# Performance work log

Measured on AMD Instinct MI355X. Metric: run time of the kernel, lower is better.

The kernel has to match this reference:

```python
import jax, jax.numpy as jnp
import numpy as np

DIM = 1024
N_HEADS = 16
HEAD_DIM = DIM // N_HEADS
SPARSITY = 0.8
SCALE = HEAD_DIM ** -0.5


def setup_inputs() -> dict:
    key = jax.random.key(0)
    ks = jax.random.split(key, 9)
    B, S = 2, 2048
    std = DIM ** -0.5
    return {
        "x": jax.random.normal(ks[0], (B, S, DIM), dtype=jnp.float32),
        "wq": jax.random.normal(ks[1], (DIM, DIM), dtype=jnp.float32) * std,
        "bq": jnp.zeros((DIM,), dtype=jnp.float32),
        "wk": jax.random.normal(ks[2], (DIM, DIM), dtype=jnp.float32) * std,
        "bk": jnp.zeros((DIM,), dtype=jnp.float32),
        "wv": jax.random.normal(ks[3], (DIM, DIM), dtype=jnp.float32) * std,
        "bv": jnp.zeros((DIM,), dtype=jnp.float32),
        "wo": jax.random.normal(ks[4], (DIM, DIM), dtype=jnp.float32) * std,
        "bo": jnp.zeros((DIM,), dtype=jnp.float32),
    }


def _attn(x, wq, bq, wk, bk, wv, bv, wo, bo):
    B, S, _ = x.shape
    # torch Linear: y = x @ W.T + b
    def proj(w, b):
        y = jnp.einsum('bsd,ed->bse', x, w) + b
        return y.reshape(B, S, N_HEADS, HEAD_DIM).transpose(0, 2, 1, 3)  # [B,H,S,hd]
    q, k, v = proj(wq, bq), proj(wk, bk), proj(wv, bv)
    scores = jnp.einsum('bhqd,bhkd->bhqk', q, k) * SCALE  # [B,H,S,S]
    # top-k sparsity: keep k = max(1, int(S*(1-sparsity))) largest per row
    kk = max(1, int(S * (1.0 - SPARSITY)))
    topk_vals, topk_idx = jax.lax.top_k(scores, kk)
    sparse = jnp.full_like(scores, -jnp.inf)
    sparse = jnp.put_along_axis(sparse, topk_idx, topk_vals, axis=-1, inplace=False)
    attn = jax.nn.softmax(sparse, axis=-1)  # dropout disabled (eval)
    out = jnp.einsum('bhqk,bhkd->bhqd', attn, v)
    out = out.transpose(0, 2, 1, 3).reshape(B, S, DIM)
    out = jnp.einsum('bsd,ed->bse', out, wo) + bo
    return out, attn


def reference(x, wq, bq, wk, bk, wv, bv, wo, bo):
    return _attn(x, wq, bq, wk, bk, wv, bv, wo, bo)
```

## Files before the change

kernel.cpp:

```cpp
#include <hip/hip_runtime.h>
#include <hip/hip_bf16.h>

#define DIMN 1024
#define NH 16
#define HD 64
#define SEQ 2048
#define BATCH 2
#define BHN (BATCH*NH)
#define MROWS (BATCH*SEQ)
#define KKEEP 409
#define SCALEF 0.125f
#define QROWS 16

typedef __attribute__((ext_vector_type(8))) short short8;
typedef __attribute__((ext_vector_type(4))) short short4v;
typedef __attribute__((ext_vector_type(4))) float f32x4;

#define MFMA(a,b,c) __builtin_amdgcn_mfma_f32_16x16x32_bf16(a,b,c,0,0,0)


static __device__ __forceinline__ short f2bf(float f) {
    __hip_bfloat16 h = __float2bfloat16(f);
    return *reinterpret_cast<short*>(&h);
}
static __device__ __forceinline__ float bf2f(short s) {
    __hip_bfloat16 h = *reinterpret_cast<__hip_bfloat16*>(&s);
    return __bfloat162float(h);
}
static __device__ __forceinline__ short8 ld8(const short* p) {
    return *reinterpret_cast<const short8*>(p);
}
static __device__ __forceinline__ float keyf(unsigned u) {
    unsigned fu = (u & 0x80000000u) ? (u ^ 0x80000000u) : ~u;
    return __uint_as_float(fu);
}
static __device__ __forceinline__ size_t tidx(int row, int k) {
    return (size_t)(row >> 4) * 16384 + (size_t)(k >> 5) * 512
         + ((((k >> 3) & 3) * 16 + (row & 15)) * 8) + (k & 7);
}

static __device__ __forceinline__ void conv_hilo_body(
    const float* in, short* hi, short* lo, int rows) {
    const int total = rows * 256;
    for (int idx = blockIdx.x * blockDim.x + threadIdx.x; idx < total;
         idx += gridDim.x * blockDim.x) {
        const int row = idx >> 8;
        const int k = (idx & 255) * 4;
        float4 v = *reinterpret_cast<const float4*>(in + (size_t)row * DIMN + k);
        short4v h, l;
        #pragma unroll
        for (int j = 0; j < 4; ++j) {
            float f = (&v.x)[j];
            short hb = f2bf(f);
            h[j] = hb;
            l[j] = f2bf(f - bf2f(hb));
        }
        const size_t o = tidx(row, k);
        *reinterpret_cast<short4v*>(hi + o) = h;
        *reinterpret_cast<short4v*>(lo + o) = l;
    }
}
static __device__ __forceinline__ void conv_bf16_body(
    const float* in, short* out, int rows) {
    const int total = rows * 256;
    for (int idx = blockIdx.x * blockDim.x + threadIdx.x; idx < total;
         idx += gridDim.x * blockDim.x) {
        const int row = idx >> 8;
        const int k = (idx & 255) * 4;
        float4 v = *reinterpret_cast<const float4*>(in + (size_t)row * DIMN + k);
        short4v o;
        o[0] = f2bf(v.x); o[1] = f2bf(v.y); o[2] = f2bf(v.z); o[3] = f2bf(v.w);
        *reinterpret_cast<short4v*>(out + tidx(row, k)) = o;
    }
}
__global__ void conv_all(
    const float* __restrict__ x, const float* __restrict__ wq,
    const float* __restrict__ wk, const float* __restrict__ wv,
    const float* __restrict__ wo,
    short* __restrict__ xhi, short* __restrict__ xlo,
    short* __restrict__ wqh, short* __restrict__ wql,
    short* __restrict__ wkh, short* __restrict__ wkl,
    short* __restrict__ wvb, short* __restrict__ wob)
{
    switch (blockIdx.y) {
        case 0: conv_hilo_body(x,  xhi, xlo, MROWS); break;
        case 1: conv_hilo_body(wq, wqh, wql, DIMN);  break;
        case 2: conv_hilo_body(wk, wkh, wkl, DIMN);  break;
        case 3: conv_bf16_body(wv, wvb, DIMN);       break;
        default: conv_bf16_body(wo, wob, DIMN);      break;
    }
}

__global__ __launch_bounds__(256) void qkv_mfma(
    const short* __restrict__ xh, const short* __restrict__ xl,
    const short* __restrict__ wqh, const short* __restrict__ wql, const float* __restrict__ bq,
    const short* __restrict__ wkh, const short* __restrict__ wkl, const float* __restrict__ bk,
    const short* __restrict__ wvb, const float* __restrict__ bv,
    short* __restrict__ qhi, short* __restrict__ qlo,
    short* __restrict__ khi, short* __restrict__ klo,
    short* __restrict__ vt)
{
    const int z = blockIdx.z;
    const int tid  = threadIdx.x;
    const int wv_  = tid >> 6, lane = tid & 63;
    const int r    = lane & 15, kg = lane >> 4;
    const int m_base = blockIdx.x * 128 + wv_ * 32;
    const int n_base = blockIdx.y * 64;
    const int mtile0 = blockIdx.x * 8 + wv_ * 2;
    const int ntile0 = blockIdx.y * 4;
    const int h = blockIdx.y;

    f32x4 acc[2][4] = {};

    if (z < 2) {
        const short* wh = z ? wkh : wqh;
        const short* wl = z ? wkl : wql;
        const float* bias = z ? bk : bq;
        short* dhi = z ? khi : qhi;
        short* dlo = z ? klo : qlo;

        for (int ks = 0; ks < 32; ++ks) {
            short8 ah0 = ld8(xh + (size_t)mtile0 * 16384 + ks * 512 + lane * 8);
            short8 al0 = ld8(xl + (size_t)mtile0 * 16384 + ks * 512 + lane * 8);
            short8 ah1 = ld8(xh + (size_t)(mtile0 + 1) * 16384 + ks * 512 + lane * 8);
            short8 al1 = ld8(xl + (size_t)(mtile0 + 1) * 16384 + ks * 512 + lane * 8);
            #pragma unroll
            for (int nf = 0; nf < 4; ++nf) {
                short8 bh = ld8(wh + (size_t)(ntile0 + nf) * 16384 + ks * 512 + lane * 8);
                short8 bl = ld8(wl + (size_t)(ntile0 + nf) * 16384 + ks * 512 + lane * 8);
                acc[0][nf] = MFMA(ah0, bh, acc[0][nf]);
                acc[0][nf] = MFMA(ah0, bl, acc[0][nf]);
                acc[0][nf] = MFMA(al0, bh, acc[0][nf]);
                acc[1][nf] = MFMA(ah1, bh, acc[1][nf]);
                acc[1][nf] = MFMA(ah1, bl, acc[1][nf]);
                acc[1][nf] = MFMA(al1, bh, acc[1][nf]);
            }
        }

        #pragma unroll
        for (int mf = 0; mf < 2; ++mf)
            #pragma unroll
            for (int nf = 0; nf < 4; ++nf)
                #pragma unroll
                for (int i = 0; i < 4; ++i) {
                    const int m  = m_base + mf * 16 + kg * 4 + i;
                    const int nn = n_base + nf * 16 + r;
                    const float val = acc[mf][nf][i] + bias[nn];
                    const int b_ = m >> 11, s = m & 2047;
                    const int hd = nf * 16 + r;
                    const size_t idx = (size_t)(b_ * NH + h) * 131072
                        + (size_t)(s >> 4) * 1024 + (hd >> 5) * 512
                        + ((((hd >> 3) & 3) * 16 + (s & 15)) * 8) + (hd & 7);
                    const short hb = f2bf(val);
                    dhi[idx] = hb;
                    dlo[idx] = f2bf(val - bf2f(hb));
                }
    } else {
        for (int ks = 0; ks < 32; ++ks) {
            short8 ah0 = ld8(xh + (size_t)mtile0 * 16384 + ks * 512 + lane * 8);
            short8 al0 = ld8(xl + (size_t)mtile0 * 16384 + ks * 512 + lane * 8);
            short8 ah1 = ld8(xh + (size_t)(mtile0 + 1) * 16384 + ks * 512 + lane * 8);
            short8 al1 = ld8(xl + (size_t)(mtile0 + 1) * 16384 + ks * 512 + lane * 8);
            #pragma unroll
            for (int nf = 0; nf < 4; ++nf) {
                short8 b = ld8(wvb + (size_t)(ntile0 + nf) * 16384 + ks * 512 + lane * 8);
                acc[0][nf] = MFMA(ah0, b, acc[0][nf]);
                acc[0][nf] = MFMA(al0, b, acc[0][nf]);
                acc[1][nf] = MFMA(ah1, b, acc[1][nf]);
                acc[1][nf] = MFMA(al1, b, acc[1][nf]);
            }
        }

        #pragma unroll
        for (int mf = 0; mf < 2; ++mf)
            #pragma unroll
            for (int nf = 0; nf < 4; ++nf)
                #pragma unroll
                for (int i = 0; i < 4; ++i) {
                    const int m  = m_base + mf * 16 + kg * 4 + i;
                    const int nn = n_base + nf * 16 + r;
                    const float val = acc[mf][nf][i] + bv[nn];
                    const int b_ = m >> 11, s = m & 2047;
                    const int hd = nf * 16 + r;
                    const size_t idx = (size_t)(b_ * NH + h) * 131072
                        + (size_t)(hd >> 4) * 32768 + (size_t)(s >> 5) * 512
                        + ((((s >> 3) & 3) * 16 + (hd & 15)) * 8) + (s & 7);
                    vt[idx] = f2bf(val);
                }
    }
}

__global__ __launch_bounds__(512, 4) void fused_attn(
    const short* __restrict__ qh, const short* __restrict__ ql,
    const short* __restrict__ kh, const short* __restrict__ kl,
    const short* __restrict__ vtb, float* __restrict__ attn,
    short* __restrict__ ctxt)
{
    __shared__ __align__(16) char smem[65536];
    float* CT = (float*)(smem + 32768);

    const int tid = threadIdx.x;
    const int w   = tid >> 6, lane = tid & 63;
    const int r   = lane & 15, kg = lane >> 4;

    const int bid  = blockIdx.x;
    const int xcd  = bid & 7;
    const int slot = bid >> 3;
    const int bh   = xcd + 8 * (slot >> 7);
    const int qt   = slot & 127;
    const int q0   = qt * QROWS;

    const size_t qtbase = (size_t)bh * 131072 + (size_t)qt * 1024 + lane * 8;
    short8 a0h = ld8(qh + qtbase),       a0l = ld8(ql + qtbase);
    short8 a1h = ld8(qh + qtbase + 512), a1l = ld8(ql + qtbase + 512);

    unsigned u[2][32];

    auto STAGE = [&](int c, float* buf) {
        #pragma unroll
        for (int tt = 0; tt < 4; ++tt) {
            const int stile = c * 32 + w + 8 * tt;
            const size_t tb = (size_t)bh * 131072 + (size_t)stile * 1024 + lane * 8;
            short8 b0h = ld8(kh + tb);
            short8 b0l = ld8(kl + tb);
            short8 b1h = ld8(kh + tb + 512);
            short8 b1l = ld8(kl + tb + 512);
            f32x4 accA = {0.f, 0.f, 0.f, 0.f};
            f32x4 accB = {0.f, 0.f, 0.f, 0.f};
            accA = MFMA(a0h, b0h, accA);
            accB = MFMA(a1h, b1h, accB);
            accA = MFMA(a0h, b0l, accA);
            accB = MFMA(a1h, b1l, accB);
            accA = MFMA(a0l, b0h, accA);
            accB = MFMA(a1l, b1h, accB);
            const int j0c = (w + 8 * tt) * 16;
            #pragma unroll
            for (int i = 0; i < 4; ++i)
                buf[(kg * 4 + i) * 512 + j0c + r] = (accA[i] + accB[i]) * SCALEF;
        }
    };

    STAGE(0, (float*)smem);
    __syncthreads();
    #pragma unroll
    for (int c = 0; c < 4; ++c) {
        float* cur = (float*)(smem + ((c & 1) ? 32768 : 0));
        float* nxt = (float*)(smem + ((c & 1) ? 0 : 32768));
        if (c + 1 < 4) STAGE(c + 1, nxt);
        #pragma unroll
        for (int rr = 0; rr < 2; ++rr) {
            const float* src = cur + (w + 8 * rr) * 512;
            #pragma unroll
            for (int g = 0; g < 2; ++g) {
                f32x4 v4 = *reinterpret_cast<const f32x4*>(src + g * 256 + lane * 4);
                #pragma unroll
                for (int q_ = 0; q_ < 4; ++q_) {
                    unsigned fu = __float_as_uint(v4[q_]);
                    u[rr][c * 8 + g * 4 + q_] =
                        (fu & 0x80000000u) ? ~fu : (fu | 0x80000000u);
                }
            }
        }
        __syncthreads();
    }

    float inv[2];
    #pragma unroll
    for (int rr = 0; rr < 2; ++rr) {
        unsigned cur = 0;
        for (int bit = 31; bit >= 0; --bit) {
            const unsigned cand = cur | (1u << bit);
            int cnt = 0;
            #pragma unroll
            for (int jj = 0; jj < 32; ++jj)
                cnt += __popcll(__ballot(u[rr][jj] >= cand));
            if (cnt >= KKEEP) {
                cur = cand;
                if (cnt == KKEEP) break;
            }
        }
        unsigned mu = 0;
        #pragma unroll
        for (int jj = 0; jj < 32; ++jj) mu = (u[rr][jj] > mu) ? u[rr][jj] : mu;
        #pragma unroll
        for (int off = 32; off; off >>= 1) {
            unsigned o = (unsigned)__shfl_xor((int)mu, off);
            mu = (o > mu) ? o : mu;
        }
        const float m = keyf(mu);
        float denom = 0.f;
        #pragma unroll
        for (int jj = 0; jj < 32; ++jj) {
            const unsigned ue = u[rr][jj];
            const float e = (ue >= cur) ? __expf(keyf(ue) - m) : 0.f;
            u[rr][jj] = __float_as_uint(e);
            denom += e;
        }
        #pragma unroll
        for (int off = 32; off; off >>= 1) denom += __shfl_xor(denom, off);
        inv[rr] = 1.0f / denom;
    }

    const int khf = w >> 2;
    const int swzw = (w & 7) << 4;
    const int swzr = (r & 7) << 4;
    f32x4 acc = {0.f, 0.f, 0.f, 0.f};

    auto EWRITE = [&](int c, char* Ebase) {
        #pragma unroll
        for (int rr = 0; rr < 2; ++rr) {
            const int row = w + 8 * rr;
            const float iv = inv[rr];
            #pragma unroll
            for (int g = 0; g < 2; ++g) {
                short4v pb;
                pb[0] = f2bf(__uint_as_float(u[rr][c * 8 + g * 4 + 0]) * iv);
                pb[1] = f2bf(__uint_as_float(u[rr][c * 8 + g * 4 + 1]) * iv);
                pb[2] = f2bf(__uint_as_float(u[rr][c * 8 + g * 4 + 2]) * iv);
                pb[3] = f2bf(__uint_as_float(u[rr][c * 8 + g * 4 + 3]) * iv);
                *reinterpret_cast<short4v*>(
                    Ebase + row * 1024 + ((g * 512 + lane * 8) ^ swzw)) = pb;
            }
        }
    };
    auto PVSTEP = [&](int c, const char* Ebase) {
        const size_t vbase = (size_t)bh * 131072 + (size_t)(w & 3) * 32768
                           + (size_t)(c * 16 + khf * 8) * 512 + lane * 8;
        const char* Eb2 = Ebase + r * 1024;
        #pragma unroll
        for (int ks = 0; ks < 8; ++ks) {
            const int kk = khf * 8 + ks;
            short8 pa = *reinterpret_cast<const short8*>(
                Eb2 + ((kk * 64 + kg * 16) ^ swzr));
            short8 vb = ld8(vtb + vbase + ks * 512);
            acc = MFMA(pa, vb, acc);
        }
    };

    EWRITE(0, smem);
    __syncthreads();
    #pragma unroll
    for (int c = 0; c < 4; ++c) {
        char* curE = smem + ((c & 1) ? 16384 : 0);
        char* nxtE = smem + ((c & 1) ? 0 : 16384);
        if (c + 1 < 4) EWRITE(c + 1, nxtE);
        PVSTEP(c, curE);
        __syncthreads();
    }

    const int dt = w & 3;
    if (khf == 1) {
        #pragma unroll
        for (int i = 0; i < 4; ++i) CT[(kg * 4 + i) * 64 + dt * 16 + r] = acc[i];
    }
    __syncthreads();
    if (khf == 0) {
        const int b_ = bh >> 4, h = bh & 15;
        const size_t base = (size_t)(b_ * 128 + qt) * 16384
                          + (size_t)(h * 2 + (dt >> 1)) * 512;
        #pragma unroll
        for (int i = 0; i < 4; ++i) {
            const int lrow = kg * 4 + i;
            const float val = acc[i] + CT[lrow * 64 + dt * 16 + r];
            ctxt[base + ((((dt * 2 + (r >> 3)) & 3) * 16 + lrow) * 8) + (r & 7)]
                = f2bf(val);
        }
    }

    #pragma unroll
    for (int rr = 0; rr < 2; ++rr) {
        const int row = w + 8 * rr;
        const float iv = inv[rr];
        float* arow = attn + ((size_t)bh * SEQ + q0 + row) * SEQ + lane * 4;
        #pragma unroll
        for (int c = 0; c < 4; ++c)
            #pragma unroll
            for (int g = 0; g < 2; ++g) {
                f32x4 pv;
                pv[0] = __uint_as_float(u[rr][c * 8 + g * 4 + 0]) * iv;
                pv[1] = __uint_as_float(u[rr][c * 8 + g * 4 + 1]) * iv;
                pv[2] = __uint_as_float(u[rr][c * 8 + g * 4 + 2]) * iv;
                pv[3] = __uint_as_float(u[rr][c * 8 + g * 4 + 3]) * iv;
                __builtin_nontemporal_store(
                    pv, reinterpret_cast<f32x4*>(arow + c * 512 + g * 256));
            }
    }
}

__global__ __launch_bounds__(256) void out_mfma(
    const short* __restrict__ ctxt, const short* __restrict__ wob,
    const float* __restrict__ bo, float* __restrict__ out)
{
    const int tid = threadIdx.x;
    const int w_  = tid >> 6, lane = tid & 63;
    const int r   = lane & 15, kg = lane >> 4;
    const int m_base = blockIdx.x * 128 + w_ * 32;
    const int n_base = blockIdx.y * 64;
    const int mtile0 = blockIdx.x * 8 + w_ * 2;
    const int ntile0 = blockIdx.y * 4;

    f32x4 acc[2][4] = {};

    for (int ks = 0; ks < 32; ++ks) {
        short8 a0 = ld8(ctxt + (size_t)mtile0 * 16384 + ks * 512 + lane * 8);
        short8 a1 = ld8(ctxt + (size_t)(mtile0 + 1) * 16384 + ks * 512 + lane * 8);
        #pragma unroll
        for (int nf = 0; nf < 4; ++nf) {
            short8 b = ld8(wob + (size_t)(ntile0 + nf) * 16384 + ks * 512 + lane * 8);
            acc[0][nf] = MFMA(a0, b, acc[0][nf]);
            acc[1][nf] = MFMA(a1, b, acc[1][nf]);
        }
    }

    #pragma unroll
    for (int mf = 0; mf < 2; ++mf)
        #pragma unroll
        for (int nf = 0; nf < 4; ++nf)
            #pragma unroll
            for (int i = 0; i < 4; ++i) {
                const int m  = m_base + mf * 16 + kg * 4 + i;
                const int nn = n_base + nf * 16 + r;
                out[(size_t)m * DIMN + nn] = acc[mf][nf][i] + bo[nn];
            }
}

extern "C" void kernel_launch(void* const* d_in, const int* in_sizes, int n_in,
                              void* d_out, int out_size, void* d_ws, size_t ws_size,
                              hipStream_t stream) {
    const float* x  = (const float*)d_in[0];
    const float* wq = (const float*)d_in[1];
    const float* bq = (const float*)d_in[2];
    const float* wk = (const float*)d_in[3];
    const float* bk = (const float*)d_in[4];
    const float* wv = (const float*)d_in[5];
    const float* bv = (const float*)d_in[6];
    const float* wo = (const float*)d_in[7];
    const float* bo = (const float*)d_in[8];

    float* out  = (float*)d_out;
    float* attn = out + (size_t)MROWS * DIMN;

    short* xhi = (short*)attn;
    short* xlo = xhi + (size_t)MROWS * DIMN;
    short* wqh = xlo + (size_t)MROWS * DIMN;
    short* wql = wqh + (size_t)DIMN * DIMN;
    short* wkh = wql + (size_t)DIMN * DIMN;
    short* wkl = wkh + (size_t)DIMN * DIMN;
    short* wvb = wkl + (size_t)DIMN * DIMN;

    const size_t QKV = (size_t)BHN * SEQ * HD;
    short* qhi = (short*)d_ws;
    short* qlo = qhi + QKV;
    short* khi = qlo + QKV;
    short* klo = khi + QKV;
    short* vt  = klo + QKV;
    short* ctx = vt  + QKV;
    short* wob = ctx + QKV;

    conv_all<<<dim3(512, 5), 256, 0, stream>>>(
        x, wq, wk, wv, wo, xhi, xlo, wqh, wql, wkh, wkl, wvb, wob);

    qkv_mfma<<<dim3(MROWS / 128, DIMN / 64, 3), 256, 0, stream>>>(
        xhi, xlo, wqh, wql, bq, wkh, wkl, bk, wvb, bv,
        qhi, qlo, khi, klo, vt);

    fused_attn<<<dim3(SEQ / QROWS * BHN), 512, 0, stream>>>(
        qhi, qlo, khi, klo, vt, attn, ctx);

    out_mfma<<<dim3(MROWS / 128, DIMN / 64), 256, 0, stream>>>(ctx, wob, bo, out);
}
```

Baseline: 408.7 us.

## Prefetch V tiles into registers and batch K loads with MFMA priority

The QK staging loop now issues the global loads for two K tiles before running their MFMAs, and raises wave priority around the MFMA bursts. V operands for the PV product are loaded into registers one chunk ahead: the first chunk is loaded before the top-k threshold search and later chunks are loaded after each PV step. The aim is to hide global load latency behind the radix-select and MFMA work. The cost is higher register pressure from the extra short8 arrays, which could lower occupancy.

Result: slower. 437.8 us (+7.1%).

```diff
diff --git a/kernel.cpp b/kernel.cpp
--- a/kernel.cpp
+++ b/kernel.cpp
@@ -218,25 +218,36 @@
 
     auto STAGE = [&](int c, float* buf) {
         #pragma unroll
-        for (int tt = 0; tt < 4; ++tt) {
-            const int stile = c * 32 + w + 8 * tt;
-            const size_t tb = (size_t)bh * 131072 + (size_t)stile * 1024 + lane * 8;
-            short8 b0h = ld8(kh + tb);
-            short8 b0l = ld8(kl + tb);
-            short8 b1h = ld8(kh + tb + 512);
-            short8 b1l = ld8(kl + tb + 512);
-            f32x4 accA = {0.f, 0.f, 0.f, 0.f};
-            f32x4 accB = {0.f, 0.f, 0.f, 0.f};
-            accA = MFMA(a0h, b0h, accA);
-            accB = MFMA(a1h, b1h, accB);
-            accA = MFMA(a0h, b0l, accA);
-            accB = MFMA(a1h, b1l, accB);
-            accA = MFMA(a0l, b0h, accA);
-            accB = MFMA(a1l, b1h, accB);
-            const int j0c = (w + 8 * tt) * 16;
-            #pragma unroll
-            for (int i = 0; i < 4; ++i)
-                buf[(kg * 4 + i) * 512 + j0c + r] = (accA[i] + accB[i]) * SCALEF;
+        for (int half = 0; half < 2; ++half) {
+            short8 L[2][4];
+            #pragma unroll
+            for (int t2 = 0; t2 < 2; ++t2) {
+                const int tt = half * 2 + t2;
+                const int stile = c * 32 + w + 8 * tt;
+                const size_t tb = (size_t)bh * 131072 + (size_t)stile * 1024 + lane * 8;
+                L[t2][0] = ld8(kh + tb);
+                L[t2][1] = ld8(kl + tb);
+                L[t2][2] = ld8(kh + tb + 512);
+                L[t2][3] = ld8(kl + tb + 512);
+            }
+            __builtin_amdgcn_s_setprio(1);
+            #pragma unroll
+            for (int t2 = 0; t2 < 2; ++t2) {
+                const int tt = half * 2 + t2;
+                f32x4 accA = {0.f, 0.f, 0.f, 0.f};
+                f32x4 accB = {0.f, 0.f, 0.f, 0.f};
+                accA = MFMA(a0h, L[t2][0], accA);
+                accB = MFMA(a1h, L[t2][2], accB);
+                accA = MFMA(a0h, L[t2][1], accA);
+                accB = MFMA(a1h, L[t2][3], accB);
+                accA = MFMA(a0l, L[t2][0], accA);
+                accB = MFMA(a1l, L[t2][2], accB);
+                const int j0c = (w + 8 * tt) * 16;
+                #pragma unroll
+                for (int i = 0; i < 4; ++i)
+                    buf[(kg * 4 + i) * 512 + j0c + r] = (accA[i] + accB[i]) * SCALEF;
+            }
+            __builtin_amdgcn_s_setprio(0);
         }
     };
 
@@ -264,6 +275,16 @@
         __syncthreads();
     }
 
+    const int khf = w >> 2;
+    short8 vr[8];
+    auto VLOAD = [&](int c) {
+        const size_t vbase = (size_t)bh * 131072 + (size_t)(w & 3) * 32768
+                           + (size_t)(c * 16 + khf * 8) * 512 + lane * 8;
+        #pragma unroll
+        for (int ks = 0; ks < 8; ++ks) vr[ks] = ld8(vtb + vbase + ks * 512);
+    };
+    VLOAD(0);
+
     float inv[2];
     #pragma unroll
     for (int rr = 0; rr < 2; ++rr) {
@@ -301,7 +322,6 @@
         inv[rr] = 1.0f / denom;
     }
 
-    const int khf = w >> 2;
     const int swzw = (w & 7) << 4;
     const int swzr = (r & 7) << 4;
     f32x4 acc = {0.f, 0.f, 0.f, 0.f};
@@ -324,17 +344,16 @@
         }
     };
     auto PVSTEP = [&](int c, const char* Ebase) {
-        const size_t vbase = (size_t)bh * 131072 + (size_t)(w & 3) * 32768
-                           + (size_t)(c * 16 + khf * 8) * 512 + lane * 8;
         const char* Eb2 = Ebase + r * 1024;
+        __builtin_amdgcn_s_setprio(1);
         #pragma unroll
         for (int ks = 0; ks < 8; ++ks) {
             const int kk = khf * 8 + ks;
             short8 pa = *reinterpret_cast<const short8*>(
                 Eb2 + ((kk * 64 + kg * 16) ^ swzr));
-            short8 vb = ld8(vtb + vbase + ks * 512);
-            acc = MFMA(pa, vb, acc);
-        }
+            acc = MFMA(pa, vr[ks], acc);
+        }
+        __builtin_amdgcn_s_setprio(0);
     };
 
     EWRITE(0, smem);
@@ -345,6 +364,7 @@
         char* nxtE = smem + ((c & 1) ? 0 : 16384);
         if (c + 1 < 4) EWRITE(c + 1, nxtE);
         PVSTEP(c, curE);
+        if (c + 1 < 4) VLOAD(c + 1);
         __syncthreads();
     }
 
```
